# Kernel tuning notes

Hardware: AMD Instinct MI355X
Metric: run time of the kernel (lower is better)

The kernel has to match this reference:

```python
import jax, jax.numpy as jnp
import numpy as np

EPS = 1e-7


def setup_inputs() -> dict:
    key = jax.random.key(0)
    k1, k2, k3 = jax.random.split(key, 3)
    N = 4194304
    risk_scores = jax.random.normal(k1, (N,), dtype=jnp.float32)
    times = jax.random.randint(k2, (N,), 0, 50000, dtype=jnp.int32)
    events = jax.random.randint(k3, (N,), 0, 2, dtype=jnp.int32)
    return {"risk_scores": risk_scores, "times": times, "events": events}


def _efron_loss(risk_scores, times, events):
    N = risk_scores.shape[0]
    # sort descending by time (stable), as in torch.argsort(times, descending=True)
    order = jnp.argsort(-times, stable=True)
    lr = risk_scores[order]          # log risk, sorted
    t = times[order]
    e = events[order]
    risk = jnp.exp(lr)
    # reversed cumsum: risk set sum for each position (suffix sum)
    csr = jnp.cumsum(risk[::-1])[::-1]
    m = (e == 1)
    mf = m.astype(lr.dtype)
    # segment id per unique time value (contiguous after sort)
    boundary = jnp.concatenate([jnp.zeros((1,), jnp.int32),
                                (t[1:] != t[:-1]).astype(jnp.int32)])
    seg = jnp.cumsum(boundary)       # [N] in [0, N)
    idx = jnp.arange(N)
    # per-segment stats over events
    n_per_seg = jax.ops.segment_sum(mf, seg, num_segments=N)            # n_events at this time
    risk_at_seg = jax.ops.segment_sum(risk * mf, seg, num_segments=N)   # sum of exp(lr) over tied events
    first_ev = jax.ops.segment_min(jnp.where(m, idx, N), seg, num_segments=N)  # event_idx[0]
    seg_start = jax.ops.segment_min(idx, seg, num_segments=N)
    # within-tie event rank j (0-based): events in this segment strictly before i
    c_excl = jnp.cumsum(mf) - mf
    j = c_excl - c_excl[seg_start[seg]]
    n_i = n_per_seg[seg]
    risk_time_i = risk_at_seg[seg]
    risk_set_i = csr[jnp.clip(first_ev[seg], 0, N - 1)]
    correction = (j / jnp.maximum(n_i, 1.0)) * risk_time_i
    per_event = jnp.log(risk_set_i - correction + EPS) - lr
    total_loss = jnp.sum(jnp.where(m, per_event, 0.0))
    total_events = jnp.sum(mf)
    return jnp.where(total_events > 0, total_loss / jnp.maximum(total_events, 1.0), 0.0)


def reference(risk_scores, times, events):
    return _efron_loss(risk_scores, times, events)
```

## Files before the change

### kernel.cpp

```cpp
#include <hip/hip_runtime.h>
#include <hip/hip_fp16.h>
#include <math.h>

#define TBINS   50000
#define NR      4
#define RBINS   12500
#define GROUP   256
#define NGROUPS 196
#define EPSF    1e-7f
#define NPB     256
#define NWV     16
#define NSL     64
#define PER_SLICE 256000

#define OFF_SCAL  0
#define OFF_NEV   16
#define OFF_DONE  20
#define OFF_GSUM  64
#define OFF_ALLG  2048
#define OFF_EVG   202048
#define OFF_CNTG  402048
#define OFF_LRP   602048
#define OFF_NP    603072
#define OFF_CNTS  604160
#define OFF_PART  669696

__global__ __launch_bounds__(1024) void k_part(
        const float* __restrict__ lr, const int* __restrict__ tm,
        const int* __restrict__ ev, int N, int WCH,
        unsigned* __restrict__ part, unsigned* __restrict__ cnts,
        float* __restrict__ lrp, int* __restrict__ np) {
    __shared__ float red_f[16];
    __shared__ int   red_i[16];
    const int b = blockIdx.x, tid = threadIdx.x;
    const int w = tid >> 6, lane = tid & 63;
    const unsigned long long lmask = (1ULL << lane) - 1ULL;

    const int base0 = (b * NWV + w) * WCH;
    const unsigned seg0 = (unsigned)(b * NWV + w) * 4u;
    unsigned wc0 = 0, wc1 = 0, wc2 = 0, wc3 = 0;
    float l_lr = 0.f; int l_n = 0;

#define PART1(L, T, E, VALID) {                                           \
        float r_ = __expf(L);                                             \
        unsigned hb_ = (unsigned)__half_as_ushort(__float2half(r_));      \
        bool ve_ = (VALID) && ((E) != 0);                                 \
        if (ve_) { hb_ |= 0x8000u; l_lr += (L); l_n++; }                  \
        unsigned P_  = ((unsigned)(T) << 16) | hb_;                       \
        unsigned rg_ = ((unsigned)(T)) / 12500u;                          \
        { unsigned long long m_ = __ballot((VALID) && rg_ == 0u);         \
          if ((VALID) && rg_ == 0u)                                       \
              part[(size_t)(seg0 + 0u) * WCH + wc0 + (unsigned)__popcll(m_ & lmask)] = P_; \
          wc0 += (unsigned)__popcll(m_); }                                \
        { unsigned long long m_ = __ballot((VALID) && rg_ == 1u);         \
          if ((VALID) && rg_ == 1u)                                       \
              part[(size_t)(seg0 + 1u) * WCH + wc1 + (unsigned)__popcll(m_ & lmask)] = P_; \
          wc1 += (unsigned)__popcll(m_); }                                \
        { unsigned long long m_ = __ballot((VALID) && rg_ == 2u);         \
          if ((VALID) && rg_ == 2u)                                       \
              part[(size_t)(seg0 + 2u) * WCH + wc2 + (unsigned)__popcll(m_ & lmask)] = P_; \
          wc2 += (unsigned)__popcll(m_); }                                \
        { unsigned long long m_ = __ballot((VALID) && rg_ == 3u);         \
          if ((VALID) && rg_ == 3u)                                       \
              part[(size_t)(seg0 + 3u) * WCH + wc3 + (unsigned)__popcll(m_ & lmask)] = P_; \
          wc3 += (unsigned)__popcll(m_); }                                \
    }

    for (int it = 0; it < WCH; it += 256) {
        int idx = base0 + it + lane * 4;
        float4 l4 = {0.f, 0.f, 0.f, 0.f};
        int4   t4 = {0, 0, 0, 0};
        int4   e4 = {0, 0, 0, 0};
        if (idx + 3 < N) {
            l4 = *(const float4*)(lr + idx);
            t4 = *(const int4*)(tm + idx);
            e4 = *(const int4*)(ev + idx);
        } else if (idx < N) {
            float* lp = (float*)&l4; int* tp = (int*)&t4; int* ep = (int*)&e4;
            for (int k = 0; k < 4 && idx + k < N; ++k) {
                lp[k] = lr[idx + k]; tp[k] = tm[idx + k]; ep[k] = ev[idx + k];
            }
        }
        PART1(l4.x, t4.x, e4.x, (idx + 0) < N)
        PART1(l4.y, t4.y, e4.y, (idx + 1) < N)
        PART1(l4.z, t4.z, e4.z, (idx + 2) < N)
        PART1(l4.w, t4.w, e4.w, (idx + 3) < N)
    }

    if (lane == 0) {
        unsigned* c = cnts + seg0;
        c[0] = wc0; c[1] = wc1; c[2] = wc2; c[3] = wc3;
    }

    #pragma unroll
    for (int off = 32; off > 0; off >>= 1) {
        l_lr += __shfl_down(l_lr, off, 64);
        l_n  += __shfl_down(l_n,  off, 64);
    }
    if (lane == 0) { red_f[w] = l_lr; red_i[w] = l_n; }
    __syncthreads();
    if (tid == 0) {
        float s = 0.f; int c = 0;
        #pragma unroll
        for (int i = 0; i < NWV; ++i) { s += red_f[i]; c += red_i[i]; }
        lrp[b] = s; np[b] = c;
    }
}

__global__ __launch_bounds__(1024) void k_pass(
        const unsigned* __restrict__ part, const unsigned* __restrict__ cnts,
        int WCH, char* __restrict__ slices) {
    __shared__ float    s_all[RBINS];
    __shared__ unsigned s_evcnt[RBINS];
    const int bid = blockIdx.x;
    const int r = bid & 3, s = bid >> 2;
    const unsigned rbase = (unsigned)(r * RBINS);
    const int tid = threadIdx.x, w = tid >> 6, lane = tid & 63;

    for (int i = tid; i < RBINS; i += 1024) { s_all[i] = 0.f; s_evcnt[i] = 0u; }
    __syncthreads();

    for (int sl = w; sl < 4 * NWV; sl += NWV) {
        int pb = 4 * s + (sl >> 4);
        int pw = sl & 15;
        unsigned seg = (unsigned)(pb * NWV + pw) * 4u + (unsigned)r;
        unsigned cnt = cnts[seg];
        const unsigned* sp = part + (size_t)seg * WCH;
        for (unsigned i = (unsigned)lane; i < cnt; i += 64u) {
            unsigned P = sp[i];
            unsigned rel = (P >> 16) - rbase;
            if (rel < (unsigned)RBINS) {
                float r_ = __half2float(__ushort_as_half((unsigned short)(P & 0x7FFFu)));
                atomicAdd(&s_all[rel], r_);
                if (P & 0x8000u) {
                    unsigned enc = (1u << 28) + (unsigned)(r_ * 65536.0f + 0.5f);
                    atomicAdd(&s_evcnt[rel], enc);
                }
            }
        }
    }
    __syncthreads();

    char* sb = slices + (size_t)s * PER_SLICE;
    unsigned*      wab = (unsigned*)sb;
    unsigned char* wcq = (unsigned char*)(sb + 200000);
    for (int i = tid; i < RBINS; i += 1024) {
        float a = s_all[i];
        unsigned ec = s_evcnt[i];
        float e = (float)(ec & 0x0FFFFFFFu) * (1.0f / 65536.0f);
        wab[rbase + i] = (unsigned)__half_as_ushort(__float2half(a))
                       | ((unsigned)__half_as_ushort(__float2half(e)) << 16);
        wcq[rbase + i] = (unsigned char)(ec >> 28);
    }
}

__global__ __launch_bounds__(256) void k_reduce(const char* __restrict__ slices,
                                                const float* __restrict__ lrp,
                                                const int* __restrict__ np,
                                                float* all_g, float* ev_g, int* cnt_g,
                                                float* gsum, double* scal, int* nev,
                                                int* done) {
    __shared__ float lds[4];
    __shared__ float ldsf2[4];
    __shared__ int   ldsi2[4];
    int tid = threadIdx.x;
    int b = blockIdx.x * 256 + tid;
    float a = 0.f, d = 0.f; int c = 0;
    if (b < TBINS) {
        for (int s = 0; s < NSL; ++s) {
            const char* sb = slices + (size_t)s * PER_SLICE;
            unsigned ab = ((const unsigned*)sb)[b];
            a += __half2float(__ushort_as_half((unsigned short)(ab & 0xFFFFu)));
            d += __half2float(__ushort_as_half((unsigned short)(ab >> 16)));
            c += ((const unsigned char*)(sb + 200000))[b];
        }
        all_g[b] = a; ev_g[b] = d; cnt_g[b] = c;
    }
    int lane = tid & 63, wv = tid >> 6;
    float v = a;
    #pragma unroll
    for (int off = 32; off > 0; off >>= 1) v += __shfl_down(v, off, 64);
    if (lane == 0) lds[wv] = v;
    __syncthreads();
    if (tid == 0) {
        float s = 0.f;
        #pragma unroll
        for (int w = 0; w < 4; ++w) s += lds[w];
        gsum[blockIdx.x] = s;
    }

    if (blockIdx.x == 0) {
        float pl = lrp[tid];
        int   pn = np[tid];
        #pragma unroll
        for (int off = 32; off > 0; off >>= 1) {
            pl += __shfl_down(pl, off, 64);
            pn += __shfl_down(pn, off, 64);
        }
        if (lane == 0) { ldsf2[wv] = pl; ldsi2[wv] = pn; }
        __syncthreads();
        if (tid == 0) {
            float s = 0.f; int n = 0;
            #pragma unroll
            for (int w = 0; w < 4; ++w) { s += ldsf2[w]; n += ldsi2[w]; }
            scal[0] = (double)s;
            scal[1] = 0.0;
            *nev    = n;
            *done   = 0;
        }
    }
}

__global__ __launch_bounds__(256) void k_loss(
        const float* __restrict__ all_g, const float* __restrict__ gsum,
        const int* __restrict__ cnt_g, const float* __restrict__ ev_g,
        double* scal, const int* __restrict__ nev, int* done,
        float* __restrict__ out) {
    __shared__ float lds_r[4];
    __shared__ float lds_s[4];
    __shared__ float sh_base;
    int b   = blockIdx.x;
    int tid = threadIdx.x;
    int t   = b * GROUP + tid;
    int lane = tid & 63, wv = tid >> 6;

    float gv = (tid < b) ? gsum[tid] : 0.f;
    float red = gv;
    #pragma unroll
    for (int off = 32; off > 0; off >>= 1) red += __shfl_down(red, off, 64);
    if (lane == 0) lds_r[wv] = red;
    __syncthreads();
    if (tid == 0) {
        float s = 0.f;
        #pragma unroll
        for (int w = 0; w < 4; ++w) s += lds_r[w];
        sh_base = s;
    }
    __syncthreads();
    float base = sh_base;

    float v = (t < TBINS) ? all_g[t] : 0.f;
    float x = v;
    #pragma unroll
    for (int off = 1; off < 64; off <<= 1) {
        float y = __shfl_up(x, off, 64);
        if (lane >= off) x += y;
    }
    if (lane == 63) lds_s[wv] = x;
    __syncthreads();
    float wb = 0.f;
    for (int w = 0; w < wv; ++w) wb += lds_s[w];
    float prefix = base + wb + (x - v);

    float acc = 0.f;
    if (t < TBINS) {
        int n = cnt_g[t];
        if (n > 0) {
            float D  = ev_g[t];
            float nf = (float)n;
            float P  = D + (v - D) * (nf / (nf + 1.f));
            float R  = prefix + P;
            for (int j = 0; j < n; ++j) {
                float arg = R - ((float)j / nf) * D + EPSF;
                acc += __logf(arg);
            }
        }
    }
    __syncthreads();
    #pragma unroll
    for (int off = 32; off > 0; off >>= 1) acc += __shfl_down(acc, off, 64);
    if (lane == 0) lds_r[wv] = acc;
    __syncthreads();
    if (tid == 0) {
        float s = 0.f;
        #pragma unroll
        for (int w = 0; w < 4; ++w) s += lds_r[w];
        atomicAdd(&scal[1], (double)s);
        __threadfence();
        int ticket = atomicAdd(done, 1);
        if (ticket == NGROUPS - 1) {
            double logsum = atomicAdd(&scal[1], 0.0);
            int n = *nev;
            out[0] = (n > 0) ? (float)((logsum - scal[0]) / (double)n) : 0.f;
        }
    }
}

extern "C" void kernel_launch(void* const* d_in, const int* in_sizes, int n_in,
                              void* d_out, int out_size, void* d_ws, size_t ws_size,
                              hipStream_t stream) {
    const float* lr = (const float*)d_in[0];
    const int*   tm = (const int*)d_in[1];
    const int*   ev = (const int*)d_in[2];
    int N = in_sizes[0];

    char*     ws    = (char*)d_ws;
    double*   scal  = (double*)(ws + OFF_SCAL);
    int*      nev   = (int*)(ws + OFF_NEV);
    int*      done  = (int*)(ws + OFF_DONE);
    float*    gsum  = (float*)(ws + OFF_GSUM);
    float*    all_g = (float*)(ws + OFF_ALLG);
    float*    ev_g  = (float*)(ws + OFF_EVG);
    int*      cnt_g = (int*)(ws + OFF_CNTG);
    float*    lrp   = (float*)(ws + OFF_LRP);
    int*      np    = (int*)(ws + OFF_NP);
    unsigned* cnts  = (unsigned*)(ws + OFF_CNTS);
    unsigned* part  = (unsigned*)(ws + OFF_PART);

    int WCH = (int)((((long long)N + (NPB * NWV) - 1) / (NPB * NWV) + 255) / 256) * 256;
    size_t part_bytes = (size_t)NPB * NWV * 4 * WCH * 4;
    char* slices = ws + OFF_PART + part_bytes;

    k_part<<<NPB, 1024, 0, stream>>>(lr, tm, ev, N, WCH, part, cnts, lrp, np);
    k_pass<<<NR * NSL, 1024, 0, stream>>>(part, cnts, WCH, slices);
    k_reduce<<<NGROUPS, 256, 0, stream>>>(slices, lrp, np, all_g, ev_g, cnt_g,
                                          gsum, scal, nev, done);
    k_loss<<<NGROUPS, 256, 0, stream>>>(all_g, gsum, cnt_g, ev_g, scal, nev, done,
                                        (float*)d_out);
}
```

Baseline: 75.14 us.

## Fuse reduce and loss kernels, halve slices, compute group sums in pass kernel

Merges the slice-reduction and loss kernels into a single final kernel that reduces 32 slices per bin and computes the Efron log terms directly, with no global intermediate arrays. Each pass block now handles 8 partition blocks instead of 4, so there are half as many slices to reduce. Per-group prefix sums are accumulated with atomics inside the pass kernel, with the zeroing moved into the partition kernel. This saves one launch and the intermediate global traffic, but gives the final kernel only 50 blocks and each pass block twice the work.

```diff
diff --git a/kernel.cpp b/kernel.cpp
--- a/kernel.cpp
+++ b/kernel.cpp
@@ -5,36 +5,40 @@
 #define TBINS   50000
 #define NR      4
 #define RBINS   12500
-#define GROUP   256
-#define NGROUPS 196
 #define EPSF    1e-7f
 #define NPB     256
 #define NWV     16
-#define NSL     64
+#define NSL     32
+#define NFB     50
+#define GROUPB  1000
 #define PER_SLICE 256000
 
 #define OFF_SCAL  0
-#define OFF_NEV   16
-#define OFF_DONE  20
+#define OFF_DONE  16
 #define OFF_GSUM  64
-#define OFF_ALLG  2048
-#define OFF_EVG   202048
-#define OFF_CNTG  402048
-#define OFF_LRP   602048
-#define OFF_NP    603072
-#define OFF_CNTS  604160
-#define OFF_PART  669696
+#define OFF_LRP   512
+#define OFF_NP    1536
+#define OFF_CNTS  4096
+#define OFF_PART  69632
 
 __global__ __launch_bounds__(1024) void k_part(
         const float* __restrict__ lr, const int* __restrict__ tm,
         const int* __restrict__ ev, int N, int WCH,
         unsigned* __restrict__ part, unsigned* __restrict__ cnts,
-        float* __restrict__ lrp, int* __restrict__ np) {
+        float* __restrict__ lrp, int* __restrict__ np,
+        float* __restrict__ gsum, double* __restrict__ scal,
+        int* __restrict__ done) {
     __shared__ float red_f[16];
     __shared__ int   red_i[16];
     const int b = blockIdx.x, tid = threadIdx.x;
     const int w = tid >> 6, lane = tid & 63;
     const unsigned long long lmask = (1ULL << lane) - 1ULL;
+
+    if (b == 0) {
+        if (tid < NFB) gsum[tid] = 0.f;
+        if (tid == NFB)     scal[1] = 0.0;
+        if (tid == NFB + 1) *done   = 0;
+    }
 
     const int base0 = (b * NWV + w) * WCH;
     const unsigned seg0 = (unsigned)(b * NWV + w) * 4u;
@@ -109,26 +113,26 @@
 
 __global__ __launch_bounds__(1024) void k_pass(
         const unsigned* __restrict__ part, const unsigned* __restrict__ cnts,
-        int WCH, char* __restrict__ slices) {
+        int WCH, char* __restrict__ slices, float* __restrict__ gsum) {
     __shared__ float    s_all[RBINS];
     __shared__ unsigned s_evcnt[RBINS];
     const int bid = blockIdx.x;
     const int r = bid & 3, s = bid >> 2;
-    const unsigned rbase = (unsigned)(r * RBINS);
+    const int rbase = r * RBINS;
     const int tid = threadIdx.x, w = tid >> 6, lane = tid & 63;
 
     for (int i = tid; i < RBINS; i += 1024) { s_all[i] = 0.f; s_evcnt[i] = 0u; }
     __syncthreads();
 
-    for (int sl = w; sl < 4 * NWV; sl += NWV) {
-        int pb = 4 * s + (sl >> 4);
+    for (int sl = w; sl < 8 * NWV; sl += NWV) {
+        int pb = 8 * s + (sl >> 4);
         int pw = sl & 15;
         unsigned seg = (unsigned)(pb * NWV + pw) * 4u + (unsigned)r;
         unsigned cnt = cnts[seg];
         const unsigned* sp = part + (size_t)seg * WCH;
         for (unsigned i = (unsigned)lane; i < cnt; i += 64u) {
             unsigned P = sp[i];
-            unsigned rel = (P >> 16) - rbase;
+            unsigned rel = (P >> 16) - (unsigned)rbase;
             if (rel < (unsigned)RBINS) {
                 float r_ = __half2float(__ushort_as_half((unsigned short)(P & 0x7FFFu)));
                 atomicAdd(&s_all[rel], r_);
@@ -152,21 +156,37 @@
                        | ((unsigned)__half_as_ushort(__float2half(e)) << 16);
         wcq[rbase + i] = (unsigned char)(ec >> 28);
     }
-}
-
-__global__ __launch_bounds__(256) void k_reduce(const char* __restrict__ slices,
-                                                const float* __restrict__ lrp,
-                                                const int* __restrict__ np,
-                                                float* all_g, float* ev_g, int* cnt_g,
-                                                float* gsum, double* scal, int* nev,
-                                                int* done) {
-    __shared__ float lds[4];
-    __shared__ float ldsf2[4];
-    __shared__ int   ldsi2[4];
-    int tid = threadIdx.x;
-    int b = blockIdx.x * 256 + tid;
+
+    int g0 = rbase / GROUPB;
+    int gN = (rbase + RBINS - 1) / GROUPB;
+    if (w <= gN - g0) {
+        int g  = g0 + w;
+        int lo = g * GROUPB;     if (lo < rbase)         lo = rbase;
+        int hi = g * GROUPB + GROUPB; if (hi > rbase + RBINS) hi = rbase + RBINS;
+        float p = 0.f;
+        for (int i = lo - rbase + lane; i < hi - rbase; i += 64)
+            p += __half2float(__float2half(s_all[i]));
+        #pragma unroll
+        for (int off = 32; off > 0; off >>= 1) p += __shfl_down(p, off, 64);
+        if (lane == 0) atomicAdd(&gsum[g], p);
+    }
+}
+
+__global__ __launch_bounds__(1024) void k_final(
+        const char* __restrict__ slices, const float* __restrict__ gsum,
+        const float* __restrict__ lrp, const int* __restrict__ np,
+        double* scal, int* done, float* __restrict__ out) {
+    __shared__ float wtot[16];
+    __shared__ float red_f[16];
+    __shared__ int   red_i[16];
+    __shared__ float sh_base;
+    __shared__ int   sh_last;
+    const int bid = blockIdx.x, tid = threadIdx.x;
+    const int w = tid >> 6, lane = tid & 63;
+    const int b = bid * GROUPB + tid;
+
     float a = 0.f, d = 0.f; int c = 0;
-    if (b < TBINS) {
+    if (tid < GROUPB) {
         for (int s = 0; s < NSL; ++s) {
             const char* sb = slices + (size_t)s * PER_SLICE;
             unsigned ab = ((const unsigned*)sb)[b];
@@ -174,114 +194,70 @@
             d += __half2float(__ushort_as_half((unsigned short)(ab >> 16)));
             c += ((const unsigned char*)(sb + 200000))[b];
         }
-        all_g[b] = a; ev_g[b] = d; cnt_g[b] = c;
-    }
-    int lane = tid & 63, wv = tid >> 6;
-    float v = a;
+    }
+
+    if (w == 0) {
+        float gg = (lane < bid) ? gsum[lane] : 0.f;
+        #pragma unroll
+        for (int off = 32; off > 0; off >>= 1) gg += __shfl_down(gg, off, 64);
+        if (lane == 0) sh_base = gg;
+    }
+
+    float x = a;
     #pragma unroll
-    for (int off = 32; off > 0; off >>= 1) v += __shfl_down(v, off, 64);
-    if (lane == 0) lds[wv] = v;
+    for (int off = 1; off < 64; off <<= 1) {
+        float y = __shfl_up(x, off, 64);
+        if (lane >= off) x += y;
+    }
+    if (lane == 63) wtot[w] = x;
+    __syncthreads();
+    float wb = 0.f;
+    for (int i = 0; i < w; ++i) wb += wtot[i];
+    float prefix = sh_base + wb + (x - a);
+
+    float acc = 0.f;
+    if (tid < GROUPB && c > 0) {
+        float D  = d;
+        float nf = (float)c;
+        float P  = D + (a - D) * (nf / (nf + 1.f));
+        float R  = prefix + P;
+        for (int j = 0; j < c; ++j) {
+            float arg = R - ((float)j / nf) * D + EPSF;
+            acc += __logf(arg);
+        }
+    }
+    #pragma unroll
+    for (int off = 32; off > 0; off >>= 1) acc += __shfl_down(acc, off, 64);
+    __syncthreads();
+    if (lane == 0) red_f[w] = acc;
     __syncthreads();
     if (tid == 0) {
         float s = 0.f;
         #pragma unroll
-        for (int w = 0; w < 4; ++w) s += lds[w];
-        gsum[blockIdx.x] = s;
-    }
-
-    if (blockIdx.x == 0) {
-        float pl = lrp[tid];
-        int   pn = np[tid];
+        for (int i = 0; i < 16; ++i) s += red_f[i];
+        atomicAdd(&scal[1], (double)s);
+        __threadfence();
+        int ticket = atomicAdd(done, 1);
+        sh_last = (ticket == NFB - 1) ? 1 : 0;
+    }
+    __syncthreads();
+
+    if (sh_last) {
+        float pl = (tid < NPB) ? lrp[tid] : 0.f;
+        int   pn = (tid < NPB) ? np[tid]  : 0;
         #pragma unroll
         for (int off = 32; off > 0; off >>= 1) {
             pl += __shfl_down(pl, off, 64);
             pn += __shfl_down(pn, off, 64);
         }
-        if (lane == 0) { ldsf2[wv] = pl; ldsi2[wv] = pn; }
+        if (lane == 0) { red_f[w] = pl; red_i[w] = pn; }
         __syncthreads();
         if (tid == 0) {
             float s = 0.f; int n = 0;
             #pragma unroll
-            for (int w = 0; w < 4; ++w) { s += ldsf2[w]; n += ldsi2[w]; }
-            scal[0] = (double)s;
-            scal[1] = 0.0;
-            *nev    = n;
-            *done   = 0;
-        }
-    }
-}
-
-__global__ __launch_bounds__(256) void k_loss(
-        const float* __restrict__ all_g, const float* __restrict__ gsum,
-        const int* __restrict__ cnt_g, const float* __restrict__ ev_g,
-        double* scal, const int* __restrict__ nev, int* done,
-        float* __restrict__ out) {
-    __shared__ float lds_r[4];
-    __shared__ float lds_s[4];
-    __shared__ float sh_base;
-    int b   = blockIdx.x;
-    int tid = threadIdx.x;
-    int t   = b * GROUP + tid;
-    int lane = tid & 63, wv = tid >> 6;
-
-    float gv = (tid < b) ? gsum[tid] : 0.f;
-    float red = gv;
-    #pragma unroll
-    for (int off = 32; off > 0; off >>= 1) red += __shfl_down(red, off, 64);
-    if (lane == 0) lds_r[wv] = red;
-    __syncthreads();
-    if (tid == 0) {
-        float s = 0.f;
-        #pragma unroll
-        for (int w = 0; w < 4; ++w) s += lds_r[w];
-        sh_base = s;
-    }
-    __syncthreads();
-    float base = sh_base;
-
-    float v = (t < TBINS) ? all_g[t] : 0.f;
-    float x = v;
-    #pragma unroll
-    for (int off = 1; off < 64; off <<= 1) {
-        float y = __shfl_up(x, off, 64);
-        if (lane >= off) x += y;
-    }
-    if (lane == 63) lds_s[wv] = x;
-    __syncthreads();
-    float wb = 0.f;
-    for (int w = 0; w < wv; ++w) wb += lds_s[w];
-    float prefix = base + wb + (x - v);
-
-    float acc = 0.f;
-    if (t < TBINS) {
-        int n = cnt_g[t];
-        if (n > 0) {
-            float D  = ev_g[t];
-            float nf = (float)n;
-            float P  = D + (v - D) * (nf / (nf + 1.f));
-            float R  = prefix + P;
-            for (int j = 0; j < n; ++j) {
-                float arg = R - ((float)j / nf) * D + EPSF;
-                acc += __logf(arg);
-            }
-        }
-    }
-    __syncthreads();
-    #pragma unroll
-    for (int off = 32; off > 0; off >>= 1) acc += __shfl_down(acc, off, 64);
-    if (lane == 0) lds_r[wv] = acc;
-    __syncthreads();
-    if (tid == 0) {
-        float s = 0.f;
-        #pragma unroll
-        for (int w = 0; w < 4; ++w) s += lds_r[w];
-        atomicAdd(&scal[1], (double)s);
-        __threadfence();
-        int ticket = atomicAdd(done, 1);
-        if (ticket == NGROUPS - 1) {
+            for (int i = 0; i < 16; ++i) { s += red_f[i]; n += red_i[i]; }
             double logsum = atomicAdd(&scal[1], 0.0);
-            int n = *nev;
-            out[0] = (n > 0) ? (float)((logsum - scal[0]) / (double)n) : 0.f;
+            out[0] = (n > 0) ? (float)((logsum - (double)s) / (double)n) : 0.f;
         }
     }
 }
@@ -296,12 +272,8 @@
 
     char*     ws    = (char*)d_ws;
     double*   scal  = (double*)(ws + OFF_SCAL);
-    int*      nev   = (int*)(ws + OFF_NEV);
     int*      done  = (int*)(ws + OFF_DONE);
     float*    gsum  = (float*)(ws + OFF_GSUM);
-    float*    all_g = (float*)(ws + OFF_ALLG);
-    float*    ev_g  = (float*)(ws + OFF_EVG);
-    int*      cnt_g = (int*)(ws + OFF_CNTG);
     float*    lrp   = (float*)(ws + OFF_LRP);
     int*      np    = (int*)(ws + OFF_NP);
     unsigned* cnts  = (unsigned*)(ws + OFF_CNTS);
@@ -311,10 +283,9 @@
     size_t part_bytes = (size_t)NPB * NWV * 4 * WCH * 4;
     char* slices = ws + OFF_PART + part_bytes;
 
-    k_part<<<NPB, 1024, 0, stream>>>(lr, tm, ev, N, WCH, part, cnts, lrp, np);
-    k_pass<<<NR * NSL, 1024, 0, stream>>>(part, cnts, WCH, slices);
-    k_reduce<<<NGROUPS, 256, 0, stream>>>(slices, lrp, np, all_g, ev_g, cnt_g,
-                                          gsum, scal, nev, done);
-    k_loss<<<NGROUPS, 256, 0, stream>>>(all_g, gsum, cnt_g, ev_g, scal, nev, done,
-                                        (float*)d_out);
-}
+    k_part<<<NPB, 1024, 0, stream>>>(lr, tm, ev, N, WCH, part, cnts, lrp, np,
+                                     gsum, scal, done);
+    k_pass<<<NR * NSL, 1024, 0, stream>>>(part, cnts, WCH, slices, gsum);
+    k_final<<<NFB, 1024, 0, stream>>>(slices, gsum, lrp, np, scal, done,
+                                      (float*)d_out);
+}
```

Result: slower. 109.6 us (+45.9%).
